# Performance work log

Measured on AMD Instinct MI355X. Metric: run time of the kernel, lower is better.

Reference implementation:

```python
import jax, jax.numpy as jnp
import numpy as np

K = 20
EPS = 1e-5
SLOPE = 0.2


def _leaky(v):
    return jnp.where(v >= 0, v, SLOPE * v)


def _instnorm(v, axes):
    # InstanceNorm with affine=False: normalize per (batch, channel) over spatial axes,
    # biased variance, eps=1e-5 (torch default).
    mean = jnp.mean(v, axis=axes, keepdims=True)
    var = jnp.mean((v - mean) ** 2, axis=axes, keepdims=True)
    return (v - mean) * jax.lax.rsqrt(var + EPS)


def _knn_idx(x, k):
    # x: [B, C, N]; returns indices of k nearest neighbors (self included), [B, N, k]
    inner = -2.0 * jnp.einsum('bcn,bcm->bnm', x, x)
    xx = jnp.sum(x * x, axis=1)                      # [B, N]
    pd = -xx[:, :, None] - inner - xx[:, None, :]    # negative squared distance
    return jax.lax.top_k(pd, k)[1]


def _edge_conv(x, w):
    # x: [B, C, N]; w: [O, 2C]. Returns [B, O, N] after max-pool over k neighbors.
    B, C, N = x.shape
    idx = _knn_idx(x, K)                              # [B, N, K]
    xt = jnp.transpose(x, (0, 2, 1))                  # [B, N, C]
    b_idx = jnp.arange(B)[:, None, None]
    nb = xt[b_idx, idx]                               # [B, N, K, C] gathered neighbors
    ctr = xt[:, :, None, :]                           # [B, N, 1, C]
    feat = jnp.concatenate([nb - ctr, jnp.broadcast_to(ctr, nb.shape)], axis=-1)
    h = jnp.einsum('oc,bnkc->bonk', w, feat)          # 1x1 conv as GEMM -> [B, O, N, K]
    h = _leaky(_instnorm(h, (2, 3)))
    return jnp.max(h, axis=-1)                        # [B, O, N]


def setup_inputs() -> dict:
    key = jax.random.key(0)
    ks = jax.random.split(key, 6)
    B, N, feat_dim = 8, 2048, 512
    return {
        'x': jax.random.normal(ks[0], (B, N, 3), dtype=jnp.float32),
        'w1': jax.random.normal(ks[1], (64, 6), dtype=jnp.float32) * 0.1,
        'w2': jax.random.normal(ks[2], (64, 128), dtype=jnp.float32) * 0.1,
        'w3': jax.random.normal(ks[3], (128, 128), dtype=jnp.float32) * 0.1,
        'w4': jax.random.normal(ks[4], (256, 256), dtype=jnp.float32) * 0.1,
        'w5': jax.random.normal(ks[5], (feat_dim, 512), dtype=jnp.float32) * 0.1,
    }


def reference(x, w1, w2, w3, w4, w5):
    xc = jnp.transpose(x, (0, 2, 1))                  # [B, 3, N]
    x1 = _edge_conv(xc, w1)                           # [B, 64, N]
    x2 = _edge_conv(x1, w2)                           # [B, 64, N]
    x3 = _edge_conv(x2, w3)                           # [B, 128, N]
    x4 = _edge_conv(x3, w4)                           # [B, 256, N]
    cat = jnp.concatenate([x1, x2, x3, x4], axis=1)   # [B, 512, N]
    h = jnp.einsum('oc,bcn->bon', w5, cat)            # conv5 (1x1 conv1d)
    feat = _leaky(_instnorm(h, (2,)))
    return feat                                       # [B, feat_dim, N]
```

## Files before the change

kernel.cpp:

```cpp
#include <hip/hip_runtime.h>
#include <math.h>

#define NPTS 2048
#define NB 8
#define KNN 20
#define EPSI 1e-5f
#define SLOPE 0.2f

typedef short bf16x8 __attribute__((ext_vector_type(8)));
typedef float f32x4 __attribute__((ext_vector_type(4)));

__device__ __forceinline__ unsigned short f2bf(float x) {
    union { float f; unsigned u; } v; v.f = x;
    unsigned r = v.u + 0x7FFF + ((v.u >> 16) & 1u);
    return (unsigned short)(r >> 16);
}
__device__ __forceinline__ float bf2f(unsigned short h) {
    union { unsigned u; float f; } v; v.u = ((unsigned)h) << 16; return v.f;
}

__device__ __forceinline__ void gl_lds16(const unsigned short* g, unsigned short* l) {
    __builtin_amdgcn_global_load_lds(
        (const __attribute__((address_space(1))) void*)g,
        (__attribute__((address_space(3))) void*)l, 16, 0, 0);
}
__device__ __forceinline__ void gl_lds16f(const float* g, float* l) {
    __builtin_amdgcn_global_load_lds(
        (const __attribute__((address_space(1))) void*)g,
        (__attribute__((address_space(3))) void*)l, 16, 0, 0);
}

__global__ __launch_bounds__(256) void transpose_kernel(const float* __restrict__ xin,
                                                        float* __restrict__ xc) {
    int g = blockIdx.x * 256 + threadIdx.x;
    int b = g / NPTS, n = g % NPTS;
    float v0 = xin[(size_t)g * 3 + 0];
    float v1 = xin[(size_t)g * 3 + 1];
    float v2 = xin[(size_t)g * 3 + 2];
    xc[((size_t)b * 3 + 0) * NPTS + n] = v0;
    xc[((size_t)b * 3 + 1) * NPTS + n] = v1;
    xc[((size_t)b * 3 + 2) * NPTS + n] = v2;
}

__global__ __launch_bounds__(256) void xx_kernel(const float* __restrict__ x, int bstride, int C,
                                                 float* __restrict__ xx) {
    int g = blockIdx.x * 256 + threadIdx.x;
    int b = g / NPTS, n = g % NPTS;
    const float* p = x + (size_t)b * bstride + n;
    float s = 0.f;
    for (int c = 0; c < C; ++c) { float v = p[(size_t)c * NPTS]; s += v * v; }
    xx[g] = s;
}


#define KNN_TILE(CT) {                                                                   \
    const int M0 = (CT) * 128;                                                           \
    _Pragma("unroll")                                                                    \
    for (int s = 0; s < 4; ++s) {                                                        \
        int f = s * 1024 + tid * 4;                                                      \
        int c = f >> 7, col = f & 127;                                                   \
        if (c < C) gl_lds16f(xb + (size_t)c * NPTS + M0 + col, &Bs[0][0][0] + f);        \
    }                                                                                    \
    float acc0 = 0.f, acc1 = 0.f, acc2 = 0.f, acc3 = 0.f;                                \
    __syncthreads();                                                                     \
    int cur = 0;                                                                         \
    for (int kidx = 0; kidx < KCH; ++kidx) {                                             \
        if (kidx + 1 < KCH) {                                                            \
            int c0n = (kidx + 1) * 32;                                                   \
            _Pragma("unroll")                                                            \
            for (int s = 0; s < 4; ++s) {                                                \
                int f = s * 1024 + tid * 4;                                              \
                int c = f >> 7, col = f & 127;                                           \
                if (c0n + c < C)                                                         \
                    gl_lds16f(xb + (size_t)(c0n + c) * NPTS + M0 + col,                  \
                              &Bs[cur ^ 1][0][0] + f);                                   \
            }                                                                            \
        }                                                                                \
        int c0 = kidx * 32;                                                              \
        int KC = min(32, C - c0);                                                        \
        for (int cc = 0; cc < KC; ++cc) {                                                \
            float a = As[c0 + cc][row];                                                  \
            float4 bv = *(const float4*)&Bs[cur][cc][colq * 4];                          \
            acc0 += a * bv.x; acc1 += a * bv.y; acc2 += a * bv.z; acc3 += a * bv.w;      \
        }                                                                                \
        __syncthreads();                                                                 \
        cur ^= 1;                                                                        \
    }                                                                                    \
    {                                                                                    \
        int cb = M0 + colq * 4;                                                          \
        float4 o;                                                                        \
        o.x = 2.f * acc0 - xr - xxb[cb + 0];                                             \
        o.y = 2.f * acc1 - xr - xxb[cb + 1];                                             \
        o.z = 2.f * acc2 - xr - xxb[cb + 2];                                             \
        o.w = 2.f * acc3 - xr - xxb[cb + 3];                                             \
        *(float4*)&pdt[row][colq * 4] = o;                                               \
    }                                                                                    \
    __syncthreads();                                                                     \
    va[2 * (CT)]     = pdt[2 * w][l];                                                    \
    va[2 * (CT) + 1] = pdt[2 * w][64 + l];                                               \
    vb[2 * (CT)]     = pdt[2 * w + 1][l];                                                \
    vb[2 * (CT) + 1] = pdt[2 * w + 1][64 + l];                                           \
    __syncthreads();                                                                     \
}

#define KNN_SELECT(VARR, ROWIDX) {                                                       \
    unsigned mask = 0u;                                                                  \
    int saved = 0;                                                                       \
    for (int t = 0; t < KNN; ++t) {                                                      \
        float best = -INFINITY; int bj = 0;                                              \
        _Pragma("unroll")                                                                \
        for (int j = 0; j < 32; ++j) {                                                   \
            bool ok = ((mask >> j) & 1u) == 0u;                                          \
            if (ok && VARR[j] > best) { best = VARR[j]; bj = j; }                        \
        }                                                                                \
        int midx = l + 64 * bj;                                                          \
        _Pragma("unroll")                                                                \
        for (int off = 32; off > 0; off >>= 1) {                                         \
            float ov = __shfl_xor(best, off);                                            \
            int om = __shfl_xor(midx, off);                                              \
            if (ov > best || (ov == best && om < midx)) { best = ov; midx = om; }        \
        }                                                                                \
        if (l == t) saved = midx;                                                        \
        if ((midx & 63) == l) mask |= 1u << (midx >> 6);                                 \
    }                                                                                    \
    if (l < KNN) idxout[((size_t)b * NPTS + R0 + (ROWIDX)) * KNN + l] = saved;           \
}

__global__ __launch_bounds__(256, 3) void knn_fused3(const float* __restrict__ x, int bstride, int C,
                                                     const float* __restrict__ xx,
                                                     int* __restrict__ idxout) {
    __shared__ float As[128][8];
    __shared__ float Bs[2][32][128];
    __shared__ float pdt[8][132];
    int b = blockIdx.y;
    int R0 = blockIdx.x * 8;
    int tid = threadIdx.x;
    int row = tid & 7, colq = tid >> 3;
    int w = tid >> 6, l = tid & 63;
    const float* xb = x + (size_t)b * bstride;
    const float* xxb = xx + (size_t)b * NPTS;

    for (int f = tid; f < C * 2; f += 256) {
        int c = f >> 1, i = (f & 1) * 4;
        *(float4*)&As[c][i] = *(const float4*)&xb[(size_t)c * NPTS + R0 + i];
    }
    float va[32], vb[32];
    int KCH = (C + 31) >> 5;
    float xr = xxb[R0 + row];

    KNN_TILE(0)  KNN_TILE(1)  KNN_TILE(2)  KNN_TILE(3)
    KNN_TILE(4)  KNN_TILE(5)  KNN_TILE(6)  KNN_TILE(7)
    KNN_TILE(8)  KNN_TILE(9)  KNN_TILE(10) KNN_TILE(11)
    KNN_TILE(12) KNN_TILE(13) KNN_TILE(14) KNN_TILE(15)

    KNN_SELECT(va, 2 * w)
    KNN_SELECT(vb, 2 * w + 1)
}

__global__ __launch_bounds__(256) void yz_gemm2(const float* __restrict__ x, int bstride, int C, int O,
                                                const float* __restrict__ w,
                                                float* __restrict__ y, float* __restrict__ z) {
    __shared__ float Xs[32][64];
    __shared__ float Wd[32][68];
    __shared__ float Wz[32][68];
    int b = blockIdx.z;
    int mbase = blockIdx.x * 64;
    int obase = blockIdx.y * 64;
    int tid = threadIdx.x;
    int nq = tid & 15, oq = tid >> 4;
    const float* xb = x + (size_t)b * bstride;
    int C2 = 2 * C;
    float accy[4][4] = {}, accz[4][4] = {};

    for (int c0 = 0; c0 < C; c0 += 32) {
        int KC = min(32, C - c0);
        for (int t = tid; t < 512; t += 256) {
            int cc = t >> 4, j4 = (t & 15) * 4;
            float4 v = make_float4(0.f, 0.f, 0.f, 0.f);
            if (cc < KC) v = *(const float4*)&xb[(size_t)(c0 + cc) * NPTS + mbase + j4];
            *(float4*)&Xs[cc][j4] = v;
        }
        for (int t = tid; t < 2048; t += 256) {
            int o = t >> 5, cc = t & 31;
            float wd = 0.f, wz = 0.f;
            if (cc < KC) {
                wd = w[(size_t)(obase + o) * C2 + c0 + cc];
                wz = w[(size_t)(obase + o) * C2 + C + c0 + cc] - wd;
            }
            Wd[cc][o] = wd; Wz[cc][o] = wz;
        }
        __syncthreads();
        for (int cc = 0; cc < KC; ++cc) {
            float xv[4], wdv[4], wzv[4];
            *(float4*)xv  = *(float4*)&Xs[cc][nq * 4];
            *(float4*)wdv = *(float4*)&Wd[cc][oq * 4];
            *(float4*)wzv = *(float4*)&Wz[cc][oq * 4];
            #pragma unroll
            for (int i = 0; i < 4; ++i)
                #pragma unroll
                for (int j = 0; j < 4; ++j) {
                    accy[i][j] += wdv[i] * xv[j];
                    accz[i][j] += wzv[i] * xv[j];
                }
        }
        __syncthreads();
    }

    #pragma unroll
    for (int i = 0; i < 4; ++i) {
        size_t off = ((size_t)b * O + obase + oq * 4 + i) * NPTS + mbase + nq * 4;
        *(float4*)&y[off] = make_float4(accy[i][0], accy[i][1], accy[i][2], accy[i][3]);
        *(float4*)&z[off] = make_float4(accz[i][0], accz[i][1], accz[i][2], accz[i][3]);
    }
}

__global__ __launch_bounds__(256) void gather_norm2(const float* __restrict__ y,
                                                    const float* __restrict__ z,
                                                    const int* __restrict__ idx,
                                                    float* __restrict__ cat, int coff, int O) {
    __shared__ float yt[NPTS][4];
    __shared__ float red[32];
    int og = blockIdx.x * 4, b = blockIdx.y;
    int tid = threadIdx.x;

    for (int n = tid; n < NPTS; n += 256) {
        float4 v;
        v.x = y[((size_t)b * O + og + 0) * NPTS + n];
        v.y = y[((size_t)b * O + og + 1) * NPTS + n];
        v.z = y[((size_t)b * O + og + 2) * NPTS + n];
        v.w = y[((size_t)b * O + og + 3) * NPTS + n];
        *(float4*)&yt[n][0] = v;
    }
    __syncthreads();

    float s1[4] = {0.f, 0.f, 0.f, 0.f}, s2[4] = {0.f, 0.f, 0.f, 0.f};
    float hm[4][8];
    for (int r = 0; r < 8; ++r) {
        int n = r * 256 + tid;
        const int* ip = idx + ((size_t)b * NPTS + n) * KNN;
        float zv[4], mx[4];
        #pragma unroll
        for (int j = 0; j < 4; ++j) {
            zv[j] = z[((size_t)b * O + og + j) * NPTS + n];
            mx[j] = -INFINITY;
        }
        #pragma unroll
        for (int k = 0; k < KNN; ++k) {
            int id = ip[k];
            float4 yv = *(float4*)&yt[id][0];
            float h0 = yv.x + zv[0]; s1[0] += h0; s2[0] += h0 * h0; mx[0] = fmaxf(mx[0], h0);
            float h1 = yv.y + zv[1]; s1[1] += h1; s2[1] += h1 * h1; mx[1] = fmaxf(mx[1], h1);
            float h2 = yv.z + zv[2]; s1[2] += h2; s2[2] += h2 * h2; mx[2] = fmaxf(mx[2], h2);
            float h3 = yv.w + zv[3]; s1[3] += h3; s2[3] += h3 * h3; mx[3] = fmaxf(mx[3], h3);
        }
        #pragma unroll
        for (int j = 0; j < 4; ++j) hm[j][r] = mx[j];
    }
    #pragma unroll
    for (int off = 32; off > 0; off >>= 1)
        #pragma unroll
        for (int j = 0; j < 4; ++j) {
            s1[j] += __shfl_xor(s1[j], off);
            s2[j] += __shfl_xor(s2[j], off);
        }
    int wv = tid >> 6, lane = tid & 63;
    if (lane == 0)
        #pragma unroll
        for (int j = 0; j < 4; ++j) { red[j * 8 + wv] = s1[j]; red[j * 8 + 4 + wv] = s2[j]; }
    __syncthreads();
    const float inv = 1.f / (float)(NPTS * KNN);
    #pragma unroll
    for (int j = 0; j < 4; ++j) {
        float S1 = red[j * 8 + 0] + red[j * 8 + 1] + red[j * 8 + 2] + red[j * 8 + 3];
        float S2 = red[j * 8 + 4] + red[j * 8 + 5] + red[j * 8 + 6] + red[j * 8 + 7];
        float mean = S1 * inv;
        float var = S2 * inv - mean * mean;
        float rs = 1.f / sqrtf(var + EPSI);
        float* dst = cat + ((size_t)b * 512 + coff + og + j) * NPTS;
        #pragma unroll
        for (int r = 0; r < 8; ++r) {
            float vv = (hm[j][r] - mean) * rs;
            dst[r * 256 + tid] = vv >= 0.f ? vv : SLOPE * vv;
        }
    }
}

__global__ __launch_bounds__(256) void w5_prep(const float* __restrict__ w5,
                                               unsigned short* __restrict__ wcat) {
    int i = blockIdx.x * 256 + threadIdx.x;
    int o = i >> 9, c = i & 511;
    float x = w5[i];
    unsigned short h = f2bf(x);
    wcat[(size_t)o * 1024 + c] = h;
    wcat[(size_t)o * 1024 + 512 + c] = f2bf(x - bf2f(h));
}

__global__ __launch_bounds__(256) void catT_prep(const float* __restrict__ cat,
                                                 unsigned short* __restrict__ ct) {
    __shared__ float t[32][33];
    int b = blockIdx.z;
    int n0 = blockIdx.x * 32, c0 = blockIdx.y * 32;
    int tx = threadIdx.x & 31, ty = threadIdx.x >> 5;
    #pragma unroll
    for (int r = 0; r < 4; ++r) {
        int ci = ty + r * 8;
        t[ci][tx] = cat[((size_t)b * 512 + c0 + ci) * NPTS + n0 + tx];
    }
    __syncthreads();
    #pragma unroll
    for (int r = 0; r < 4; ++r) {
        int ni = ty + r * 8;
        float x = t[tx][ni];
        unsigned short h = f2bf(x);
        size_t off = ((size_t)b * NPTS + n0 + ni) * 1024 + c0 + tx;
        ct[off] = h;
        ct[off + 512] = f2bf(x - bf2f(h));
    }
}

__global__ __launch_bounds__(256, 2) void final_gemm_mfma2(const unsigned short* __restrict__ wcat,
                                                           const unsigned short* __restrict__ ct,
                                                           float* __restrict__ h) {
    __shared__ unsigned short smem[4 * 8192];
    int b = blockIdx.z;
    int nbase = blockIdx.x * 128, obase = blockIdx.y * 128;
    int tid = threadIdx.x;
    int w = tid >> 6, l = tid & 63;
    int wr = (w >> 1) * 64, wc = (w & 1) * 64;
    int lr = l & 15, lq = l >> 4;

    const unsigned short* Ag = wcat + (size_t)obase * 1024;
    const unsigned short* Bg = ct + ((size_t)b * NPTS + nbase) * 1024;

    int rw = l >> 3, g = l & 7, sg = g ^ rw;

    f32x4 acc[4][4] = {};

    auto STAGE = [&](int buf, int k0) {
        unsigned short* Ad = smem + buf * 16384;
        unsigned short* Bd = Ad + 8192;
        #pragma unroll
        for (int pass = 0; pass < 4; ++pass) {
            int rbase = pass * 32 + w * 8;
            int row = rbase + rw;
            gl_lds16(Ag + (size_t)row * 1024 + k0 + sg * 8, Ad + rbase * 64);
            gl_lds16(Bg + (size_t)row * 1024 + k0 + sg * 8, Bd + rbase * 64);
        }
    };

    STAGE(0, 0);
    __syncthreads();

    int cur = 0;
    for (int kt = 0; kt < 16; ++kt) {
        if (kt < 15) STAGE(cur ^ 1, (kt + 1) * 64);
        const unsigned short* As = smem + cur * 16384;
        const unsigned short* Bs = As + 8192;
        #pragma unroll
        for (int kk = 0; kk < 2; ++kk) {
            bf16x8 af[4], bf[4];
            int gl = kk * 4 + lq;
            #pragma unroll
            for (int mi = 0; mi < 4; ++mi) {
                int row = wr + mi * 16 + lr;
                af[mi] = *(const bf16x8*)&As[row * 64 + ((gl ^ (row & 7)) * 8)];
            }
            #pragma unroll
            for (int ni = 0; ni < 4; ++ni) {
                int row = wc + ni * 16 + lr;
                bf[ni] = *(const bf16x8*)&Bs[row * 64 + ((gl ^ (row & 7)) * 8)];
            }
            #pragma unroll
            for (int mi = 0; mi < 4; ++mi)
                #pragma unroll
                for (int ni = 0; ni < 4; ++ni)
                    acc[mi][ni] = __builtin_amdgcn_mfma_f32_16x16x32_bf16(af[mi], bf[ni], acc[mi][ni], 0, 0, 0);
        }
        __syncthreads();
        cur ^= 1;
    }

    int orow0 = obase + wr + lq * 4;
    int ncol0 = nbase + wc + lr;
    #pragma unroll
    for (int mi = 0; mi < 4; ++mi)
        #pragma unroll
        for (int r = 0; r < 4; ++r)
            #pragma unroll
            for (int ni = 0; ni < 4; ++ni)
                h[((size_t)b * 512 + orow0 + mi * 16 + r) * NPTS + ncol0 + ni * 16] = acc[mi][ni][r];
}

__global__ __launch_bounds__(256) void final_norm(const float* __restrict__ h,
                                                  float* __restrict__ out) {
    __shared__ float red[8];
    int o = blockIdx.x, b = blockIdx.y;
    int tid = threadIdx.x;
    const float* hr = h + ((size_t)b * 512 + o) * NPTS;
    float s1 = 0.f, s2 = 0.f;
    float v[8];
    #pragma unroll
    for (int r = 0; r < 8; ++r) {
        v[r] = hr[r * 256 + tid];
        s1 += v[r]; s2 += v[r] * v[r];
    }
    #pragma unroll
    for (int off = 32; off > 0; off >>= 1) {
        s1 += __shfl_xor(s1, off);
        s2 += __shfl_xor(s2, off);
    }
    int wv = tid >> 6, lane = tid & 63;
    if (lane == 0) { red[wv] = s1; red[4 + wv] = s2; }
    __syncthreads();
    float S1 = red[0] + red[1] + red[2] + red[3];
    float S2 = red[4] + red[5] + red[6] + red[7];
    const float inv = 1.f / (float)NPTS;
    float mean = S1 * inv;
    float var = S2 * inv - mean * mean;
    float rs = 1.f / sqrtf(var + EPSI);
    float* dst = out + ((size_t)b * 512 + o) * NPTS;
    #pragma unroll
    for (int r = 0; r < 8; ++r) {
        float vv = (v[r] - mean) * rs;
        dst[r * 256 + tid] = vv >= 0.f ? vv : SLOPE * vv;
    }
}

extern "C" void kernel_launch(void* const* d_in, const int* in_sizes, int n_in,
                              void* d_out, int out_size, void* d_ws, size_t ws_size,
                              hipStream_t stream) {
    const float* x_in = (const float*)d_in[0];
    const float* w1 = (const float*)d_in[1];
    const float* w2 = (const float*)d_in[2];
    const float* w3 = (const float*)d_in[3];
    const float* w4 = (const float*)d_in[4];
    const float* w5 = (const float*)d_in[5];
    float* out = (float*)d_out;
    float* ws = (float*)d_ws;

    float* region = ws;
    float* yb = region;
    float* zb = region + 4194304;
    int* idxb = (int*)(ws + 8388608);
    float* xxb = ws + 8388608 + 327680;
    float* xcb = xxb + NB * NPTS;
    float* cat = xcb + NB * 3 * NPTS;
    unsigned short* wcat = (unsigned short*)(cat + 8388608);
    unsigned short* ct = (unsigned short*)region;
    float* hb = cat;

    transpose_kernel<<<NB * NPTS / 256, 256, 0, stream>>>(x_in, xcb);
    w5_prep<<<512 * 512 / 256, 256, 0, stream>>>(w5, wcat);

    const float* srcs[4] = {xcb, cat, cat + (size_t)64 * NPTS, cat + (size_t)128 * NPTS};
    int bstr[4] = {3 * NPTS, 512 * NPTS, 512 * NPTS, 512 * NPTS};
    int Cin[4] = {3, 64, 64, 128};
    int Oc[4] = {64, 64, 128, 256};
    const float* wl[4] = {w1, w2, w3, w4};
    int coffs[4] = {0, 64, 128, 256};

    for (int li = 0; li < 4; ++li) {
        xx_kernel<<<NB * NPTS / 256, 256, 0, stream>>>(srcs[li], bstr[li], Cin[li], xxb);
        knn_fused3<<<dim3(NPTS / 8, NB), 256, 0, stream>>>(srcs[li], bstr[li], Cin[li], xxb, idxb);
        yz_gemm2<<<dim3(NPTS / 64, Oc[li] / 64, NB), 256, 0, stream>>>(
            srcs[li], bstr[li], Cin[li], Oc[li], wl[li], yb, zb);
        gather_norm2<<<dim3(Oc[li] / 4, NB), 256, 0, stream>>>(yb, zb, idxb, cat, coffs[li], Oc[li]);
    }

    catT_prep<<<dim3(NPTS / 32, 512 / 32, NB), 256, 0, stream>>>(cat, ct);
    final_gemm_mfma2<<<dim3(NPTS / 128, 512 / 128, NB), 256, 0, stream>>>(wcat, ct, hb);
    final_norm<<<dim3(512, NB), 256, 0, stream>>>(hb, out);
}
```

Baseline: 1.452 ms.

## Replace buffered kNN selection with streaming wave-wide top-k insertion

Instead of keeping all 32 distance values per lane in registers and doing a 20-round argmax over them at the end, each 128-column tile now feeds a running top-20 list held across lanes. Distances and column indices are packed into 64-bit sortable keys, and only candidates above the current 20th-best key are inserted, using ballot and shuffles. This drops the 64-float register arrays, which lets the launch bound rise to 4 blocks per CU for more occupancy. The cost is a data-dependent serial insertion loop with 64-bit shuffles per tile, plus a final ordering pass. Ties are still broken toward the lower index.

```diff
diff --git a/kernel.cpp b/kernel.cpp
--- a/kernel.cpp
+++ b/kernel.cpp
@@ -52,6 +52,79 @@
     xx[g] = s;
 }
 
+
+__device__ __forceinline__ unsigned long long pdkey(float v, int gcol) {
+    unsigned s = __float_as_uint(v);
+    unsigned ov = (s & 0x80000000u) ? ~s : (s | 0x80000000u);
+    return ((unsigned long long)ov << 32) | (unsigned)(~(unsigned)gcol);
+}
+
+__device__ __forceinline__ void boot20(unsigned long long k0, unsigned long long k1, int l,
+                                       unsigned long long& skey, unsigned long long& minkey) {
+    bool u0 = false, u1 = false;
+    unsigned long long bk = 0;
+    for (int t = 0; t < KNN; ++t) {
+        unsigned long long cand = 0;
+        if (!u0) cand = k0;
+        if (!u1 && k1 > cand) cand = k1;
+        bk = cand;
+        #pragma unroll
+        for (int off = 32; off > 0; off >>= 1) {
+            unsigned long long o = __shfl_xor(bk, off);
+            if (o > bk) bk = o;
+        }
+        if (l == t) skey = bk;
+        if (cand == bk && bk != 0) {
+            if (!u0 && k0 == bk) u0 = true; else u1 = true;
+        }
+    }
+    minkey = bk;
+}
+
+__device__ __forceinline__ void insert20(unsigned long long k0, unsigned long long k1, int l,
+                                         unsigned long long& skey, unsigned long long& minkey) {
+    unsigned long long b0 = __ballot(k0 > minkey);
+    unsigned long long b1 = __ballot(k1 > minkey);
+    while (b0 | b1) {
+        unsigned long long ck;
+        if (b0) { int src = __builtin_ctzll(b0); b0 &= b0 - 1; ck = __shfl(k0, src); }
+        else    { int src = __builtin_ctzll(b1); b1 &= b1 - 1; ck = __shfl(k1, src); }
+        if (ck <= minkey) continue;
+        unsigned long long mk = (l < KNN) ? skey : ~0ull;
+        int ml = l;
+        #pragma unroll
+        for (int off = 32; off > 0; off >>= 1) {
+            unsigned long long ok = __shfl_xor(mk, off);
+            int ol = __shfl_xor(ml, off);
+            if (ok < mk) { mk = ok; ml = ol; }
+        }
+        if (l == ml) skey = ck;
+        unsigned long long m2 = (l < KNN) ? skey : ~0ull;
+        #pragma unroll
+        for (int off = 32; off > 0; off >>= 1) {
+            unsigned long long o = __shfl_xor(m2, off);
+            if (o < m2) m2 = o;
+        }
+        minkey = m2;
+    }
+}
+
+__device__ __forceinline__ void emit20(int l, unsigned long long skey, int* __restrict__ dst) {
+    bool alive = (l < KNN);
+    unsigned long long out = 0;
+    for (int t = 0; t < KNN; ++t) {
+        unsigned long long cand = alive ? skey : 0;
+        unsigned long long bk = cand;
+        #pragma unroll
+        for (int off = 32; off > 0; off >>= 1) {
+            unsigned long long o = __shfl_xor(bk, off);
+            if (o > bk) bk = o;
+        }
+        if (l == t) out = bk;
+        if (alive && skey == bk) alive = false;
+    }
+    if (l < KNN) dst[l] = (int)~(unsigned)out;
+}
 
 #define KNN_TILE(CT) {                                                                   \
     const int M0 = (CT) * 128;                                                           \
@@ -96,37 +169,23 @@
         *(float4*)&pdt[row][colq * 4] = o;                                               \
     }                                                                                    \
     __syncthreads();                                                                     \
-    va[2 * (CT)]     = pdt[2 * w][l];                                                    \
-    va[2 * (CT) + 1] = pdt[2 * w][64 + l];                                               \
-    vb[2 * (CT)]     = pdt[2 * w + 1][l];                                                \
-    vb[2 * (CT) + 1] = pdt[2 * w + 1][64 + l];                                           \
+    {                                                                                    \
+        unsigned long long kA0 = pdkey(pdt[2 * w][l],      M0 + l);                      \
+        unsigned long long kA1 = pdkey(pdt[2 * w][64 + l], M0 + 64 + l);                 \
+        unsigned long long kB0 = pdkey(pdt[2 * w + 1][l],      M0 + l);                  \
+        unsigned long long kB1 = pdkey(pdt[2 * w + 1][64 + l], M0 + 64 + l);             \
+        if ((CT) == 0) {                                                                 \
+            boot20(kA0, kA1, l, skA, mkA);                                               \
+            boot20(kB0, kB1, l, skB, mkB);                                               \
+        } else {                                                                         \
+            insert20(kA0, kA1, l, skA, mkA);                                             \
+            insert20(kB0, kB1, l, skB, mkB);                                             \
+        }                                                                                \
+    }                                                                                    \
     __syncthreads();                                                                     \
 }
 
-#define KNN_SELECT(VARR, ROWIDX) {                                                       \
-    unsigned mask = 0u;                                                                  \
-    int saved = 0;                                                                       \
-    for (int t = 0; t < KNN; ++t) {                                                      \
-        float best = -INFINITY; int bj = 0;                                              \
-        _Pragma("unroll")                                                                \
-        for (int j = 0; j < 32; ++j) {                                                   \
-            bool ok = ((mask >> j) & 1u) == 0u;                                          \
-            if (ok && VARR[j] > best) { best = VARR[j]; bj = j; }                        \
-        }                                                                                \
-        int midx = l + 64 * bj;                                                          \
-        _Pragma("unroll")                                                                \
-        for (int off = 32; off > 0; off >>= 1) {                                         \
-            float ov = __shfl_xor(best, off);                                            \
-            int om = __shfl_xor(midx, off);                                              \
-            if (ov > best || (ov == best && om < midx)) { best = ov; midx = om; }        \
-        }                                                                                \
-        if (l == t) saved = midx;                                                        \
-        if ((midx & 63) == l) mask |= 1u << (midx >> 6);                                 \
-    }                                                                                    \
-    if (l < KNN) idxout[((size_t)b * NPTS + R0 + (ROWIDX)) * KNN + l] = saved;           \
-}
-
-__global__ __launch_bounds__(256, 3) void knn_fused3(const float* __restrict__ x, int bstride, int C,
+__global__ __launch_bounds__(256, 4) void knn_fused4(const float* __restrict__ x, int bstride, int C,
                                                      const float* __restrict__ xx,
                                                      int* __restrict__ idxout) {
     __shared__ float As[128][8];
@@ -144,17 +203,17 @@
         int c = f >> 1, i = (f & 1) * 4;
         *(float4*)&As[c][i] = *(const float4*)&xb[(size_t)c * NPTS + R0 + i];
     }
-    float va[32], vb[32];
     int KCH = (C + 31) >> 5;
     float xr = xxb[R0 + row];
+    unsigned long long skA = 0, skB = 0, mkA = 0, mkB = 0;
 
     KNN_TILE(0)  KNN_TILE(1)  KNN_TILE(2)  KNN_TILE(3)
     KNN_TILE(4)  KNN_TILE(5)  KNN_TILE(6)  KNN_TILE(7)
     KNN_TILE(8)  KNN_TILE(9)  KNN_TILE(10) KNN_TILE(11)
     KNN_TILE(12) KNN_TILE(13) KNN_TILE(14) KNN_TILE(15)
 
-    KNN_SELECT(va, 2 * w)
-    KNN_SELECT(vb, 2 * w + 1)
+    emit20(l, skA, idxout + ((size_t)b * NPTS + R0 + 2 * w) * KNN);
+    emit20(l, skB, idxout + ((size_t)b * NPTS + R0 + 2 * w + 1) * KNN);
 }
 
 __global__ __launch_bounds__(256) void yz_gemm2(const float* __restrict__ x, int bstride, int C, int O,
@@ -461,7 +520,7 @@
 
     for (int li = 0; li < 4; ++li) {
         xx_kernel<<<NB * NPTS / 256, 256, 0, stream>>>(srcs[li], bstr[li], Cin[li], xxb);
-        knn_fused3<<<dim3(NPTS / 8, NB), 256, 0, stream>>>(srcs[li], bstr[li], Cin[li], xxb, idxb);
+        knn_fused4<<<dim3(NPTS / 8, NB), 256, 0, stream>>>(srcs[li], bstr[li], Cin[li], xxb, idxb);
         yz_gemm2<<<dim3(NPTS / 64, Oc[li] / 64, NB), 256, 0, stream>>>(
             srcs[li], bstr[li], Cin[li], Oc[li], wl[li], yb, zb);
         gather_norm2<<<dim3(Oc[li] / 4, NB), 256, 0, stream>>>(yb, zb, idxb, cat, coffs[li], Oc[li]);
```

Measured after the change: 2.867 ms. 97.4% more time.
